# Kernel tuning notes

Hardware: AMD Instinct MI355X
Metric: run time of the kernel (lower is better)

Reference implementation:

```python
import jax, jax.numpy as jnp
import numpy as np

DIL = (1, 2, 4, 8)  # dilations, num_dilation = 4
KS = 3              # kernel_size
EPS = 1e-5


def _unfold3(x, r):
    """nn.Unfold(3, dilation=r, padding=r): x [B,d,H,W] -> [B,d,9,H*W]."""
    B, d, H, W = x.shape
    xp = jnp.pad(x, ((0, 0), (0, 0), (r, r), (r, r)))
    cols = jnp.stack([xp[:, :, i * r:i * r + H, j * r:j * r + W]
                      for i in range(KS) for j in range(KS)], axis=2)
    return cols.reshape(B, d, KS * KS, H * W)


def setup_inputs() -> dict:
    key = jax.random.key(0)
    ks = jax.random.split(key, 8)
    B, C, H, W = 8, 256, 80, 80
    s = 0.05
    return {
        "x": jax.random.normal(ks[0], (B, C, H, W), jnp.float32),
        "qkv_w": jax.random.normal(ks[1], (3 * C, C), jnp.float32) * s,
        "qkv_b": jnp.zeros((3 * C,), jnp.float32),
        "fc_w": jax.random.normal(ks[2], (4, 4), jnp.float32) * 0.3,
        "fc_b": jnp.zeros((4,), jnp.float32),
        "ln_g": jnp.ones((C // 4,), jnp.float32),
        "ln_b": jnp.zeros((C // 4,), jnp.float32),
        "proj_w": jax.random.normal(ks[3], (C, C), jnp.float32) * s,
        "proj_b": jnp.zeros((C,), jnp.float32),
        "w1": jax.random.normal(ks[4], (2 * C, C), jnp.float32) * s,
        "bn1_g": jnp.ones((2 * C,), jnp.float32),
        "bn1_b": jnp.zeros((2 * C,), jnp.float32),
        "bn1_m": jnp.zeros((2 * C,), jnp.float32),
        "bn1_v": jnp.ones((2 * C,), jnp.float32),
        "w2": jax.random.normal(ks[5], (C, 2 * C), jnp.float32) * s,
        "bn2_g": jnp.ones((C,), jnp.float32),
        "bn2_b": jnp.zeros((C,), jnp.float32),
        "bn2_m": jnp.zeros((C,), jnp.float32),
        "bn2_v": jnp.ones((C,), jnp.float32),
    }


def _bn(z, g, b, m, v):
    # BatchNorm2d, eval mode (running stats), z is [B,C,H,W]
    inv = g / jnp.sqrt(v + EPS)
    return z * inv[None, :, None, None] + (b - m * inv)[None, :, None, None]


def _psablock(x, qkv_w, qkv_b, fc_w, fc_b, ln_g, ln_b, proj_w, proj_b,
              w1, bn1_g, bn1_b, bn1_m, bn1_v, w2, bn2_g, bn2_b, bn2_m, bn2_v):
    B, C, H, W = x.shape
    ND = len(DIL)
    Cd = C // ND                  # channels per dilation branch
    num_heads = 4
    hd = C // num_heads           # head_dim = 64
    nh = Cd // hd                 # heads per branch (= 1)
    scale = hd ** -0.5

    # qkv 1x1 conv: [B,3C,H,W] -> (3, ND, Cd) split
    qkv = jnp.einsum('bchw,oc->bohw', x, qkv_w) + qkv_b[None, :, None, None]
    qkv = qkv.reshape(B, 3, ND, Cd, H, W)

    feats = []
    for i, r in enumerate(DIL):
        q, k, v = qkv[:, 0, i], qkv[:, 1, i], qkv[:, 2, i]
        qh = q.reshape(B, nh, hd, H * W)                       # [B,nh,hd,N]
        kh = _unfold3(k, r).reshape(B, nh, hd, KS * KS, H * W)  # [B,nh,hd,9,N]
        vh = _unfold3(v, r).reshape(B, nh, hd, KS * KS, H * W)
        attn = jax.nn.softmax(
            jnp.einsum('bhcn,bhcjn->bhnj', qh, kh) * scale, axis=-1)
        out = jnp.einsum('bhnj,bhcjn->bnhc', attn, vh)          # [B,N,nh,hd]
        feats.append(out.reshape(B, H, W, Cd))

    # CrossScaleFusion: Linear over scale dim + residual + LayerNorm over Cd
    stacked = jnp.stack(feats, axis=3)                          # [B,H,W,S,Cd]
    fused = jnp.einsum('bhwsc,ts->bhwtc', stacked, fc_w) \
        + fc_b[None, None, None, :, None]
    fused = fused + stacked
    mu = fused.mean(-1, keepdims=True)
    var = fused.var(-1, keepdims=True)
    normed = (fused - mu) / jnp.sqrt(var + EPS) * ln_g + ln_b

    y2 = normed.reshape(B, H, W, C)
    y3 = jnp.einsum('bhwc,oc->bhwo', y2, proj_w) + proj_b
    attn_out = y3.transpose(0, 3, 1, 2)                         # [B,C,H,W]

    x1 = x + attn_out                                           # shortcut

    # FFN: Conv1x1(C->2C)+BN+SiLU, Conv1x1(2C->C)+BN, residual
    h = jnp.einsum('bchw,oc->bohw', x1, w1)
    h = jax.nn.silu(_bn(h, bn1_g, bn1_b, bn1_m, bn1_v))
    h = jnp.einsum('bchw,oc->bohw', h, w2)
    h = _bn(h, bn2_g, bn2_b, bn2_m, bn2_v)
    return x1 + h


def reference(x, qkv_w, qkv_b, fc_w, fc_b, ln_g, ln_b, proj_w, proj_b,
              w1, bn1_g, bn1_b, bn1_m, bn1_v, w2, bn2_g, bn2_b, bn2_m, bn2_v):
    return _psablock(x, qkv_w, qkv_b, fc_w, fc_b, ln_g, ln_b, proj_w, proj_b,
                     w1, bn1_g, bn1_b, bn1_m, bn1_v,
                     w2, bn2_g, bn2_b, bn2_m, bn2_v)
```

## Files before the change

kernel.cpp:

```cpp
#include <hip/hip_runtime.h>

#define EPS_F 1e-5f

typedef __attribute__((ext_vector_type(8))) short short8;
typedef __attribute__((ext_vector_type(4))) float f32x4;
typedef __attribute__((ext_vector_type(4))) unsigned short ushort4v;
typedef __attribute__((address_space(1))) void gvoid;
typedef __attribute__((address_space(3))) void svoid;

__device__ __forceinline__ float bf2f(unsigned short u){
    union { unsigned int i; float f; } v; v.i = ((unsigned int)u) << 16; return v.f;
}
__device__ __forceinline__ unsigned short f2bf(float f){
    union { float f; unsigned int i; } v; v.f = f;
    unsigned int r = v.i + 0x7FFFu + ((v.i >> 16) & 1u);
    return (unsigned short)(r >> 16);
}

template<int EPI>
__global__ __launch_bounds__(256, 2)
void mm_k(const short* __restrict__ A, const short* __restrict__ Bt,
          const int M, const int K,
          const float* __restrict__ p0, const float* __restrict__ p1,
          const float* __restrict__ p2, const float* __restrict__ p3,
          const float* __restrict__ resid,
          short* __restrict__ outT, float* __restrict__ outF)
{
    const int N = 6400;
    __shared__ short lsA[128 * 64];
    __shared__ short lsB[128 * 64];

    const int id = blockIdx.x;
    const int b  = id & 7;
    const int rr = id >> 3;
    const int n0 = (rr % 50) * 128;
    const int m0 = (rr / 50) * 128;
    const int t  = threadIdx.x;
    const int l  = t & 63;
    const int w  = t >> 6;
    const int wr = w >> 1, wc = w & 1;

    const short* Bb = Bt + (size_t)b * N * K;

    f32x4 acc[4][4];
    #pragma unroll
    for (int i = 0; i < 4; ++i)
        #pragma unroll
        for (int j = 0; j < 4; ++j) acc[i][j] = (f32x4){0.f, 0.f, 0.f, 0.f};

    const int rsub = l >> 3;
    const int csub = l & 7;

    for (int k0 = 0; k0 < K; k0 += 64) {
        #pragma unroll
        for (int q = 0; q < 4; ++q) {
            const int row = (w * 4 + q) * 8 + rsub;
            const int cs  = csub ^ (row & 7);
            const short* ga = A  + (size_t)(m0 + row) * K + k0 + (cs << 3);
            __builtin_amdgcn_global_load_lds((gvoid*)ga, (svoid*)(lsA + (w * 4 + q) * 512), 16, 0, 0);
            const short* gb = Bb + (size_t)(n0 + row) * K + k0 + (cs << 3);
            __builtin_amdgcn_global_load_lds((gvoid*)gb, (svoid*)(lsB + (w * 4 + q) * 512), 16, 0, 0);
        }
        __syncthreads();

        #pragma unroll
        for (int ks = 0; ks < 2; ++ks) {
            short8 av[4], bv[4];
            const int cfr = ks * 4 + (l >> 4);
            #pragma unroll
            for (int mi = 0; mi < 4; ++mi) {
                const int row = wr * 64 + mi * 16 + (l & 15);
                av[mi] = *(const short8*)&lsA[row * 64 + ((cfr ^ (row & 7)) << 3)];
            }
            #pragma unroll
            for (int ni = 0; ni < 4; ++ni) {
                const int row = wc * 64 + ni * 16 + (l & 15);
                bv[ni] = *(const short8*)&lsB[row * 64 + ((cfr ^ (row & 7)) << 3)];
            }
            #pragma unroll
            for (int mi = 0; mi < 4; ++mi)
                #pragma unroll
                for (int ni = 0; ni < 4; ++ni)
                    acc[mi][ni] = __builtin_amdgcn_mfma_f32_16x16x32_bf16(
                        av[mi], bv[ni], acc[mi][ni], 0, 0, 0);
        }
        __syncthreads();
    }

    const int mq = (l >> 4) * 4;
    const int nq = l & 15;
    #pragma unroll
    for (int mi = 0; mi < 4; ++mi) {
        const int mb = m0 + wr * 64 + mi * 16 + mq;
        float mul[4], add[4];
        #pragma unroll
        for (int j = 0; j < 4; ++j) {
            const int m = mb + j;
            if (EPI == 0 || EPI == 1) { mul[j] = 1.f; add[j] = p0[m]; }
            else { const float inv = p0[m] * rsqrtf(p3[m] + EPS_F);
                   mul[j] = inv; add[j] = p1[m] - p2[m] * inv; }
        }
        #pragma unroll
        for (int ni = 0; ni < 4; ++ni) {
            const int n = n0 + wc * 64 + ni * 16 + nq;
            float z[4];
            #pragma unroll
            for (int j = 0; j < 4; ++j) {
                z[j] = acc[mi][ni][j] * mul[j] + add[j];
                if (EPI == 2) z[j] = z[j] / (1.f + __expf(-z[j]));
                if (EPI == 1 || EPI == 3)
                    z[j] += resid[((size_t)b * M + mb + j) * N + n];
            }
            if (EPI == 0 || EPI == 1 || EPI == 2) {
                ushort4v u;
                #pragma unroll
                for (int j = 0; j < 4; ++j) u[j] = f2bf(z[j]);
                *(ushort4v*)&outT[((size_t)b * N + n) * M + mb] = u;
            }
            if (EPI == 1 || EPI == 3) {
                #pragma unroll
                for (int j = 0; j < 4; ++j)
                    outF[((size_t)b * M + mb + j) * N + n] = z[j];
            }
        }
    }
}

__global__ __launch_bounds__(256, 4)
void attn_k(const short* __restrict__ qkvt,
            const float* __restrict__ fc_w, const float* __restrict__ fc_b,
            const float* __restrict__ ln_g, const float* __restrict__ ln_b,
            short* __restrict__ y2t)
{
    __shared__ short st[4][16][64];

    const int id  = blockIdx.x;
    const int b   = id & 7;
    const int hw0 = (id >> 3) * 16;
    const int t   = threadIdx.x;
    const int px  = t & 15;
    const int cg  = (t >> 4) & 3;
    const int di  = t >> 6;
    const int hw  = hw0 + px;
    const int yy  = hw / 80;
    const int xx  = hw % 80;
    const int r   = 1 << di;

    int   off[9];
    float okf[9];
    #pragma unroll
    for (int jy = 0; jy < 3; ++jy)
        #pragma unroll
        for (int jx = 0; jx < 3; ++jx) {
            const int ny = yy + (jy - 1) * r;
            const int nx = xx + (jx - 1) * r;
            const bool o = (ny >= 0) && (ny < 80) && (nx >= 0) && (nx < 80);
            okf[jy * 3 + jx] = o ? 1.f : 0.f;
            off[jy * 3 + jx] = o ? (ny * 80 + nx) : hw;
        }

    const short* base = qkvt + (size_t)b * 6400 * 768;
    const int ch = di * 64 + cg * 16;

    const short8 qv0 = *(const short8*)(base + (size_t)hw * 768 + ch);
    const short8 qv1 = *(const short8*)(base + (size_t)hw * 768 + ch + 8);
    float qf[16];
    #pragma unroll
    for (int u = 0; u < 8; ++u) { qf[u] = bf2f((unsigned short)qv0[u]);
                                  qf[8 + u] = bf2f((unsigned short)qv1[u]); }

    float s[9];
    #pragma unroll
    for (int j = 0; j < 9; ++j) {
        const short* kp = base + (size_t)off[j] * 768 + 256 + ch;
        const short8 k0 = *(const short8*)kp;
        const short8 k1 = *(const short8*)(kp + 8);
        float a = 0.f;
        #pragma unroll
        for (int u = 0; u < 8; ++u) {
            a = fmaf(qf[u],     bf2f((unsigned short)k0[u]), a);
            a = fmaf(qf[8 + u], bf2f((unsigned short)k1[u]), a);
        }
        s[j] = a;
    }

    #pragma unroll
    for (int j = 0; j < 9; ++j) {
        s[j] += __shfl_xor(s[j], 16, 64);
        s[j] += __shfl_xor(s[j], 32, 64);
        s[j] *= okf[j] * 0.125f;
    }

    float mx = s[0];
    #pragma unroll
    for (int j = 1; j < 9; ++j) mx = fmaxf(mx, s[j]);
    float e[9], sum = 0.f;
    #pragma unroll
    for (int j = 0; j < 9; ++j) { e[j] = __expf(s[j] - mx); sum += e[j]; }
    const float isum = 1.f / sum;
    float pe[9];
    #pragma unroll
    for (int j = 0; j < 9; ++j) pe[j] = e[j] * isum * okf[j];

    float o[16];
    #pragma unroll
    for (int u = 0; u < 16; ++u) o[u] = 0.f;
    #pragma unroll
    for (int j = 0; j < 9; ++j) {
        const short* vp = base + (size_t)off[j] * 768 + 512 + ch;
        const short8 v0 = *(const short8*)vp;
        const short8 v1 = *(const short8*)(vp + 8);
        #pragma unroll
        for (int u = 0; u < 8; ++u) {
            o[u]     = fmaf(pe[j], bf2f((unsigned short)v0[u]), o[u]);
            o[8 + u] = fmaf(pe[j], bf2f((unsigned short)v1[u]), o[8 + u]);
        }
    }
    short8 ov0, ov1;
    #pragma unroll
    for (int u = 0; u < 8; ++u) { ov0[u] = (short)f2bf(o[u]);
                                  ov1[u] = (short)f2bf(o[8 + u]); }
    short* sp = &st[di][px][0];
    *(short8*)(sp + (((cg * 2)     ^ (px & 7)) << 3)) = ov0;
    *(short8*)(sp + (((cg * 2 + 1) ^ (px & 7)) << 3)) = ov1;
    __syncthreads();

    float cw[4];
    #pragma unroll
    for (int s4 = 0; s4 < 4; ++s4) cw[s4] = fc_w[di * 4 + s4] + (s4 == di ? 1.f : 0.f);
    const float fb = fc_b[di];

    const int cc0 = ((cg * 2)     ^ (px & 7)) << 3;
    const int cc1 = ((cg * 2 + 1) ^ (px & 7)) << 3;
    float f[16];
    #pragma unroll
    for (int u = 0; u < 16; ++u) f[u] = fb;
    #pragma unroll
    for (int s4 = 0; s4 < 4; ++s4) {
        const short8 a0 = *(const short8*)(&st[s4][px][0] + cc0);
        const short8 a1 = *(const short8*)(&st[s4][px][0] + cc1);
        #pragma unroll
        for (int u = 0; u < 8; ++u) {
            f[u]     = fmaf(cw[s4], bf2f((unsigned short)a0[u]), f[u]);
            f[8 + u] = fmaf(cw[s4], bf2f((unsigned short)a1[u]), f[8 + u]);
        }
    }
    float mu = 0.f, sq = 0.f;
    #pragma unroll
    for (int u = 0; u < 16; ++u) { mu += f[u]; sq = fmaf(f[u], f[u], sq); }
    mu += __shfl_xor(mu, 16, 64);  mu += __shfl_xor(mu, 32, 64);
    sq += __shfl_xor(sq, 16, 64);  sq += __shfl_xor(sq, 32, 64);
    mu *= (1.f / 64.f);
    const float var  = sq * (1.f / 64.f) - mu * mu;
    const float rstd = rsqrtf(var + EPS_F);

    short* yo = y2t + ((size_t)(b * 6400 + hw)) * 256 + ch;
    short8 y0, y1;
    #pragma unroll
    for (int u = 0; u < 8; ++u) {
        const int c0 = cg * 16 + u, c1 = cg * 16 + 8 + u;
        y0[u] = (short)f2bf((f[u]     - mu) * rstd * ln_g[c0] + ln_b[c0]);
        y1[u] = (short)f2bf((f[8 + u] - mu) * rstd * ln_g[c1] + ln_b[c1]);
    }
    *(short8*)yo       = y0;
    *(short8*)(yo + 8) = y1;
}

__global__ void xt_k(const float* __restrict__ x, short* __restrict__ xt)
{
    const int b  = blockIdx.y;
    const int hw = blockIdx.x * 256 + threadIdx.x;
    const float* xb = x + (size_t)b * 256 * 6400 + hw;
    short* o = xt + ((size_t)b * 6400 + hw) * 256;
    #pragma unroll 4
    for (int c8 = 0; c8 < 32; ++c8) {
        short8 v;
        #pragma unroll
        for (int u = 0; u < 8; ++u)
            v[u] = (short)f2bf(xb[(size_t)(c8 * 8 + u) * 6400]);
        *(short8*)&o[c8 * 8] = v;
    }
}

__global__ void wc_k(const float* __restrict__ a, const float* __restrict__ bb,
                     const float* __restrict__ c, const float* __restrict__ d,
                     short* __restrict__ o)
{
    const int i = blockIdx.x * 256 + threadIdx.x;
    float v;
    if      (i < 196608)  v = a[i];
    else if (i < 262144)  v = bb[i - 196608];
    else if (i < 393216)  v = c[i - 262144];
    else                  v = d[i - 393216];
    o[i] = (short)f2bf(v);
}

extern "C" void kernel_launch(void* const* d_in, const int* in_sizes, int n_in,
                              void* d_out, int out_size, void* d_ws, size_t ws_size,
                              hipStream_t stream)
{
    const float* x      = (const float*)d_in[0];
    const float* qkv_w  = (const float*)d_in[1];
    const float* qkv_b  = (const float*)d_in[2];
    const float* fc_w   = (const float*)d_in[3];
    const float* fc_b   = (const float*)d_in[4];
    const float* ln_g   = (const float*)d_in[5];
    const float* ln_b   = (const float*)d_in[6];
    const float* proj_w = (const float*)d_in[7];
    const float* proj_b = (const float*)d_in[8];
    const float* w1     = (const float*)d_in[9];
    const float* bn1_g  = (const float*)d_in[10];
    const float* bn1_b  = (const float*)d_in[11];
    const float* bn1_m  = (const float*)d_in[12];
    const float* bn1_v  = (const float*)d_in[13];
    const float* w2     = (const float*)d_in[14];
    const float* bn2_g  = (const float*)d_in[15];
    const float* bn2_b  = (const float*)d_in[16];
    const float* bn2_m  = (const float*)d_in[17];
    const float* bn2_v  = (const float*)d_in[18];
    float* out = (float*)d_out;

    const int B = 8;

    char* ws = (char*)d_ws;
    short* wqkvb  = (short*)(ws + 0);
    short* wprojb = wqkvb + 196608;
    short* w1b    = wprojb + 65536;
    short* w2b    = w1b + 131072;
    short* xt     = (short*)(ws + 1048576);
    short* qkvt   = (short*)(ws + 27262976);
    short* y2t    = (short*)(ws + 105906176);
    short* x1t    = (short*)(ws + 132120576);
    float* x1f    = (float*)(ws + 158334976);
    short* h      = qkvt;

    dim3 blk(256);

    wc_k<<<dim3(2048), blk, 0, stream>>>(qkv_w, proj_w, w1, w2, wqkvb);

    xt_k<<<dim3(25, B), blk, 0, stream>>>(x, xt);

    mm_k<0><<<dim3(50 * 6 * 8), blk, 0, stream>>>(
        wqkvb, xt, 768, 256, qkv_b, nullptr, nullptr, nullptr, nullptr,
        qkvt, nullptr);

    attn_k<<<dim3(3200), blk, 0, stream>>>(qkvt, fc_w, fc_b, ln_g, ln_b, y2t);

    mm_k<1><<<dim3(50 * 2 * 8), blk, 0, stream>>>(
        wprojb, y2t, 256, 256, proj_b, nullptr, nullptr, nullptr, x,
        x1t, x1f);

    mm_k<2><<<dim3(50 * 4 * 8), blk, 0, stream>>>(
        w1b, x1t, 512, 256, bn1_g, bn1_b, bn1_m, bn1_v, nullptr,
        h, nullptr);

    mm_k<3><<<dim3(50 * 2 * 8), blk, 0, stream>>>(
        w2b, h, 256, 512, bn2_g, bn2_b, bn2_m, bn2_v, x1f,
        nullptr, out);
}
```

Baseline: 381.7 us.

## Fuse projection GEMM and residual into attention kernel, raise GEMM occupancy

```diff
diff --git a/kernel.cpp b/kernel.cpp
--- a/kernel.cpp
+++ b/kernel.cpp
@@ -18,7 +18,7 @@
 }
 
 template<int EPI>
-__global__ __launch_bounds__(256, 2)
+__global__ __launch_bounds__(256, 3)
 void mm_k(const short* __restrict__ A, const short* __restrict__ Bt,
           const int M, const int K,
           const float* __restrict__ p0, const float* __restrict__ p1,
@@ -96,7 +96,7 @@
         #pragma unroll
         for (int j = 0; j < 4; ++j) {
             const int m = mb + j;
-            if (EPI == 0 || EPI == 1) { mul[j] = 1.f; add[j] = p0[m]; }
+            if (EPI == 0) { mul[j] = 1.f; add[j] = p0[m]; }
             else { const float inv = p0[m] * rsqrtf(p3[m] + EPS_F);
                    mul[j] = inv; add[j] = p1[m] - p2[m] * inv; }
         }
@@ -108,16 +108,16 @@
             for (int j = 0; j < 4; ++j) {
                 z[j] = acc[mi][ni][j] * mul[j] + add[j];
                 if (EPI == 2) z[j] = z[j] / (1.f + __expf(-z[j]));
-                if (EPI == 1 || EPI == 3)
+                if (EPI == 3)
                     z[j] += resid[((size_t)b * M + mb + j) * N + n];
             }
-            if (EPI == 0 || EPI == 1 || EPI == 2) {
+            if (EPI == 0 || EPI == 2) {
                 ushort4v u;
                 #pragma unroll
                 for (int j = 0; j < 4; ++j) u[j] = f2bf(z[j]);
                 *(ushort4v*)&outT[((size_t)b * N + n) * M + mb] = u;
             }
-            if (EPI == 1 || EPI == 3) {
+            if (EPI == 3) {
                 #pragma unroll
                 for (int j = 0; j < 4; ++j)
                     outF[((size_t)b * M + mb + j) * N + n] = z[j];
@@ -127,12 +127,15 @@
 }
 
 __global__ __launch_bounds__(256, 4)
-void attn_k(const short* __restrict__ qkvt,
-            const float* __restrict__ fc_w, const float* __restrict__ fc_b,
-            const float* __restrict__ ln_g, const float* __restrict__ ln_b,
-            short* __restrict__ y2t)
+void atp_k(const short* __restrict__ qkvt,
+           const float* __restrict__ fc_w, const float* __restrict__ fc_b,
+           const float* __restrict__ ln_g, const float* __restrict__ ln_b,
+           const short* __restrict__ wproj, const float* __restrict__ proj_b,
+           const float* __restrict__ x,
+           short* __restrict__ x1t, float* __restrict__ x1f)
 {
     __shared__ short st[4][16][64];
+    __shared__ short y2s[16][256];
 
     const int id  = blockIdx.x;
     const int b   = id & 7;
@@ -183,7 +186,6 @@
         }
         s[j] = a;
     }
-
     #pragma unroll
     for (int j = 0; j < 9; ++j) {
         s[j] += __shfl_xor(s[j], 16, 64);
@@ -254,7 +256,6 @@
     const float var  = sq * (1.f / 64.f) - mu * mu;
     const float rstd = rsqrtf(var + EPS_F);
 
-    short* yo = y2t + ((size_t)(b * 6400 + hw)) * 256 + ch;
     short8 y0, y1;
     #pragma unroll
     for (int u = 0; u < 8; ++u) {
@@ -262,8 +263,49 @@
         y0[u] = (short)f2bf((f[u]     - mu) * rstd * ln_g[c0] + ln_b[c0]);
         y1[u] = (short)f2bf((f[8 + u] - mu) * rstd * ln_g[c1] + ln_b[c1]);
     }
-    *(short8*)yo       = y0;
-    *(short8*)(yo + 8) = y1;
+    {
+        const int cwb = di * 8 + cg * 2;
+        short* yr = &y2s[px][0];
+        *(short8*)(yr + (((cwb)     ^ (px & 7)) << 3)) = y0;
+        *(short8*)(yr + (((cwb + 1) ^ (px & 7)) << 3)) = y1;
+    }
+    __syncthreads();
+
+    const int wv = di;
+    const int kq = (t >> 4) & 3;
+    f32x4 pacc[4];
+    #pragma unroll
+    for (int mi = 0; mi < 4; ++mi) pacc[mi] = (f32x4){0.f, 0.f, 0.f, 0.f};
+
+    #pragma unroll
+    for (int kst = 0; kst < 8; ++kst) {
+        const short8 bY = *(const short8*)&y2s[px][(((kst * 4 + kq) ^ (px & 7)) << 3)];
+        #pragma unroll
+        for (int mi = 0; mi < 4; ++mi) {
+            const int om = wv * 64 + mi * 16 + px;
+            const short8 aW = *(const short8*)&wproj[(size_t)om * 256 + kst * 32 + kq * 8];
+            pacc[mi] = __builtin_amdgcn_mfma_f32_16x16x32_bf16(aW, bY, pacc[mi], 0, 0, 0);
+        }
+    }
+
+    #pragma unroll
+    for (int mi = 0; mi < 4; ++mi) {
+        const int ob = wv * 64 + mi * 16 + kq * 4;
+        float z[4];
+        #pragma unroll
+        for (int j = 0; j < 4; ++j) {
+            const int oc = ob + j;
+            z[j] = pacc[mi][j] + proj_b[oc]
+                 + x[((size_t)(b * 256 + oc)) * 6400 + hw];
+        }
+        ushort4v u;
+        #pragma unroll
+        for (int j = 0; j < 4; ++j) u[j] = f2bf(z[j]);
+        *(ushort4v*)&x1t[((size_t)(b * 6400 + hw)) * 256 + ob] = u;
+        #pragma unroll
+        for (int j = 0; j < 4; ++j)
+            x1f[((size_t)(b * 256 + ob + j)) * 6400 + hw] = z[j];
+    }
 }
 
 __global__ void xt_k(const float* __restrict__ x, short* __restrict__ xt)
@@ -329,7 +371,6 @@
     short* w2b    = w1b + 131072;
     short* xt     = (short*)(ws + 1048576);
     short* qkvt   = (short*)(ws + 27262976);
-    short* y2t    = (short*)(ws + 105906176);
     short* x1t    = (short*)(ws + 132120576);
     float* x1f    = (float*)(ws + 158334976);
     short* h      = qkvt;
@@ -344,11 +385,8 @@
         wqkvb, xt, 768, 256, qkv_b, nullptr, nullptr, nullptr, nullptr,
         qkvt, nullptr);
 
-    attn_k<<<dim3(3200), blk, 0, stream>>>(qkvt, fc_w, fc_b, ln_g, ln_b, y2t);
-
-    mm_k<1><<<dim3(50 * 2 * 8), blk, 0, stream>>>(
-        wprojb, y2t, 256, 256, proj_b, nullptr, nullptr, nullptr, x,
-        x1t, x1f);
+    atp_k<<<dim3(3200), blk, 0, stream>>>(qkvt, fc_w, fc_b, ln_g, ln_b,
+                                          wprojb, proj_b, x, x1t, x1f);
 
     mm_k<2><<<dim3(50 * 4 * 8), blk, 0, stream>>>(
         w1b, x1t, 512, 256, bn1_g, bn1_b, bn1_m, bn1_v, nullptr,
```

Result: slower. 390.8 us (+2.4%).

## Double-buffer B tiles in LDS and load A fragments directly to registers

Applied to the files above, without the earlier changes.

```diff
diff --git a/kernel.cpp b/kernel.cpp
--- a/kernel.cpp
+++ b/kernel.cpp
@@ -16,19 +16,24 @@
     unsigned int r = v.i + 0x7FFFu + ((v.i >> 16) & 1u);
     return (unsigned short)(r >> 16);
 }
-
-template<int EPI>
-__global__ __launch_bounds__(256, 2)
-void mm_k(const short* __restrict__ A, const short* __restrict__ Bt,
-          const int M, const int K,
+__device__ __forceinline__ void blockbar() {
+    __builtin_amdgcn_sched_barrier(0);
+    __builtin_amdgcn_s_barrier();
+    __builtin_amdgcn_sched_barrier(0);
+}
+
+template<int EPI, int KS>
+__global__ __launch_bounds__(256, 3)
+void ga_k(const short* __restrict__ A, const short* __restrict__ Bt,
+          const int M,
           const float* __restrict__ p0, const float* __restrict__ p1,
           const float* __restrict__ p2, const float* __restrict__ p3,
           const float* __restrict__ resid,
           short* __restrict__ outT, float* __restrict__ outF)
 {
     const int N = 6400;
-    __shared__ short lsA[128 * 64];
-    __shared__ short lsB[128 * 64];
+    const int K = KS * 64;
+    __shared__ short lsB[2][128 * 64];
 
     const int id = blockIdx.x;
     const int b  = id & 7;
@@ -41,50 +46,68 @@
     const int wr = w >> 1, wc = w & 1;
 
     const short* Bb = Bt + (size_t)b * N * K;
-
-    f32x4 acc[4][4];
-    #pragma unroll
-    for (int i = 0; i < 4; ++i)
-        #pragma unroll
-        for (int j = 0; j < 4; ++j) acc[i][j] = (f32x4){0.f, 0.f, 0.f, 0.f};
-
     const int rsub = l >> 3;
     const int csub = l & 7;
 
-    for (int k0 = 0; k0 < K; k0 += 64) {
+    auto stageB = [&](int k, int bufi) {
         #pragma unroll
         for (int q = 0; q < 4; ++q) {
             const int row = (w * 4 + q) * 8 + rsub;
             const int cs  = csub ^ (row & 7);
-            const short* ga = A  + (size_t)(m0 + row) * K + k0 + (cs << 3);
-            __builtin_amdgcn_global_load_lds((gvoid*)ga, (svoid*)(lsA + (w * 4 + q) * 512), 16, 0, 0);
-            const short* gb = Bb + (size_t)(n0 + row) * K + k0 + (cs << 3);
-            __builtin_amdgcn_global_load_lds((gvoid*)gb, (svoid*)(lsB + (w * 4 + q) * 512), 16, 0, 0);
-        }
-        __syncthreads();
-
+            const short* gb = Bb + (size_t)(n0 + row) * K + k * 64 + (cs << 3);
+            __builtin_amdgcn_global_load_lds((gvoid*)gb,
+                (svoid*)(&lsB[bufi][(w * 4 + q) * 512]), 16, 0, 0);
+        }
+    };
+
+    const short* Aw = A + (size_t)(m0 + wr * 64 + (l & 15)) * K + ((l >> 4) << 3);
+    short8 areg[2][2][4];
+    auto loadA = [&](int k, int pb) {
+        #pragma unroll
+        for (int ks = 0; ks < 2; ++ks)
+            #pragma unroll
+            for (int mi = 0; mi < 4; ++mi)
+                areg[pb][ks][mi] =
+                    *(const short8*)(Aw + (size_t)mi * 16 * K + k * 64 + ks * 32);
+    };
+
+    f32x4 acc[4][4];
+    #pragma unroll
+    for (int i = 0; i < 4; ++i)
+        #pragma unroll
+        for (int j = 0; j < 4; ++j) acc[i][j] = (f32x4){0.f, 0.f, 0.f, 0.f};
+
+    loadA(0, 0);
+    stageB(0, 0);
+    stageB(1, 1);
+    asm volatile("s_waitcnt vmcnt(4)" ::: "memory");
+    blockbar();
+
+    #pragma unroll
+    for (int k = 0; k < KS; ++k) {
+        if (k + 1 < KS) loadA(k + 1, (k + 1) & 1);
         #pragma unroll
         for (int ks = 0; ks < 2; ++ks) {
-            short8 av[4], bv[4];
+            short8 bv[4];
             const int cfr = ks * 4 + (l >> 4);
-            #pragma unroll
-            for (int mi = 0; mi < 4; ++mi) {
-                const int row = wr * 64 + mi * 16 + (l & 15);
-                av[mi] = *(const short8*)&lsA[row * 64 + ((cfr ^ (row & 7)) << 3)];
-            }
             #pragma unroll
             for (int ni = 0; ni < 4; ++ni) {
                 const int row = wc * 64 + ni * 16 + (l & 15);
-                bv[ni] = *(const short8*)&lsB[row * 64 + ((cfr ^ (row & 7)) << 3)];
+                bv[ni] = *(const short8*)&lsB[k & 1][row * 64 + ((cfr ^ (row & 7)) << 3)];
             }
             #pragma unroll
             for (int mi = 0; mi < 4; ++mi)
                 #pragma unroll
                 for (int ni = 0; ni < 4; ++ni)
                     acc[mi][ni] = __builtin_amdgcn_mfma_f32_16x16x32_bf16(
-                        av[mi], bv[ni], acc[mi][ni], 0, 0, 0);
-        }
-        __syncthreads();
+                        areg[k & 1][ks][mi], bv[ni], acc[mi][ni], 0, 0, 0);
+        }
+        blockbar();
+        if (k + 2 < KS) stageB(k + 2, k & 1);
+        if (k + 1 < KS) {
+            asm volatile("s_waitcnt vmcnt(4)" ::: "memory");
+            blockbar();
+        }
     }
 
     const int mq = (l >> 4) * 4;
@@ -183,7 +206,6 @@
         }
         s[j] = a;
     }
-
     #pragma unroll
     for (int j = 0; j < 9; ++j) {
         s[j] += __shfl_xor(s[j], 16, 64);
@@ -340,21 +362,21 @@
 
     xt_k<<<dim3(25, B), blk, 0, stream>>>(x, xt);
 
-    mm_k<0><<<dim3(50 * 6 * 8), blk, 0, stream>>>(
-        wqkvb, xt, 768, 256, qkv_b, nullptr, nullptr, nullptr, nullptr,
+    ga_k<0, 4><<<dim3(50 * 6 * 8), blk, 0, stream>>>(
+        wqkvb, xt, 768, qkv_b, nullptr, nullptr, nullptr, nullptr,
         qkvt, nullptr);
 
     attn_k<<<dim3(3200), blk, 0, stream>>>(qkvt, fc_w, fc_b, ln_g, ln_b, y2t);
 
-    mm_k<1><<<dim3(50 * 2 * 8), blk, 0, stream>>>(
-        wprojb, y2t, 256, 256, proj_b, nullptr, nullptr, nullptr, x,
+    ga_k<1, 4><<<dim3(50 * 2 * 8), blk, 0, stream>>>(
+        wprojb, y2t, 256, proj_b, nullptr, nullptr, nullptr, x,
         x1t, x1f);
 
-    mm_k<2><<<dim3(50 * 4 * 8), blk, 0, stream>>>(
-        w1b, x1t, 512, 256, bn1_g, bn1_b, bn1_m, bn1_v, nullptr,
+    ga_k<2, 4><<<dim3(50 * 4 * 8), blk, 0, stream>>>(
+        w1b, x1t, 512, bn1_g, bn1_b, bn1_m, bn1_v, nullptr,
         h, nullptr);
 
-    mm_k<3><<<dim3(50 * 2 * 8), blk, 0, stream>>>(
-        w2b, h, 256, 512, bn2_g, bn2_b, bn2_m, bn2_v, x1f,
+    ga_k<3, 8><<<dim3(50 * 2 * 8), blk, 0, stream>>>(
+        w2b, h, 256, bn2_g, bn2_b, bn2_m, bn2_v, x1f,
         nullptr, out);
 }
```

Result: slower. 410.7 us (+7.6%).

## Double-buffer GEMM LDS tiles with K-step 32 and fully unrolled K loop

Applied to the files above, without the earlier changes.

```diff
diff --git a/kernel.cpp b/kernel.cpp
--- a/kernel.cpp
+++ b/kernel.cpp
@@ -17,18 +17,19 @@
     return (unsigned short)(r >> 16);
 }
 
-template<int EPI>
-__global__ __launch_bounds__(256, 2)
-void mm_k(const short* __restrict__ A, const short* __restrict__ Bt,
-          const int M, const int K,
-          const float* __restrict__ p0, const float* __restrict__ p1,
-          const float* __restrict__ p2, const float* __restrict__ p3,
-          const float* __restrict__ resid,
-          short* __restrict__ outT, float* __restrict__ outF)
+template<int EPI, int KS>
+__global__ __launch_bounds__(256, 3)
+void mm2_k(const short* __restrict__ A, const short* __restrict__ Bt,
+           const int M,
+           const float* __restrict__ p0, const float* __restrict__ p1,
+           const float* __restrict__ p2, const float* __restrict__ p3,
+           const float* __restrict__ resid,
+           short* __restrict__ outT, float* __restrict__ outF)
 {
     const int N = 6400;
-    __shared__ short lsA[128 * 64];
-    __shared__ short lsB[128 * 64];
+    const int K = KS * 32;
+    __shared__ short lsA[2][128 * 32];
+    __shared__ short lsB[2][128 * 32];
 
     const int id = blockIdx.x;
     const int b  = id & 7;
@@ -42,40 +43,47 @@
 
     const short* Bb = Bt + (size_t)b * N * K;
 
+    const int srow = t >> 2;
+    const int schk = t & 3;
+
+    auto stage = [&](int k, int bufi) {
+        #pragma unroll
+        for (int q = 0; q < 2; ++q) {
+            const int row = srow + q * 64;
+            const int cs  = schk ^ (row & 3);
+            const short* ga = A  + (size_t)(m0 + row) * K + k * 32 + (cs << 3);
+            __builtin_amdgcn_global_load_lds((gvoid*)ga,
+                (svoid*)(&lsA[bufi][t * 8 + q * 2048]), 16, 0, 0);
+            const short* gb = Bb + (size_t)(n0 + row) * K + k * 32 + (cs << 3);
+            __builtin_amdgcn_global_load_lds((gvoid*)gb,
+                (svoid*)(&lsB[bufi][t * 8 + q * 2048]), 16, 0, 0);
+        }
+    };
+
     f32x4 acc[4][4];
     #pragma unroll
     for (int i = 0; i < 4; ++i)
         #pragma unroll
         for (int j = 0; j < 4; ++j) acc[i][j] = (f32x4){0.f, 0.f, 0.f, 0.f};
 
-    const int rsub = l >> 3;
-    const int csub = l & 7;
-
-    for (int k0 = 0; k0 < K; k0 += 64) {
-        #pragma unroll
-        for (int q = 0; q < 4; ++q) {
-            const int row = (w * 4 + q) * 8 + rsub;
-            const int cs  = csub ^ (row & 7);
-            const short* ga = A  + (size_t)(m0 + row) * K + k0 + (cs << 3);
-            __builtin_amdgcn_global_load_lds((gvoid*)ga, (svoid*)(lsA + (w * 4 + q) * 512), 16, 0, 0);
-            const short* gb = Bb + (size_t)(n0 + row) * K + k0 + (cs << 3);
-            __builtin_amdgcn_global_load_lds((gvoid*)gb, (svoid*)(lsB + (w * 4 + q) * 512), 16, 0, 0);
-        }
-        __syncthreads();
-
-        #pragma unroll
-        for (int ks = 0; ks < 2; ++ks) {
+    stage(0, 0);
+    __syncthreads();
+
+    #pragma unroll
+    for (int k = 0; k < KS; ++k) {
+        if (k + 1 < KS) stage(k + 1, (k + 1) & 1);
+        {
             short8 av[4], bv[4];
-            const int cfr = ks * 4 + (l >> 4);
+            const int cfr = l >> 4;
             #pragma unroll
             for (int mi = 0; mi < 4; ++mi) {
                 const int row = wr * 64 + mi * 16 + (l & 15);
-                av[mi] = *(const short8*)&lsA[row * 64 + ((cfr ^ (row & 7)) << 3)];
+                av[mi] = *(const short8*)&lsA[k & 1][row * 32 + ((cfr ^ (row & 3)) << 3)];
             }
             #pragma unroll
             for (int ni = 0; ni < 4; ++ni) {
                 const int row = wc * 64 + ni * 16 + (l & 15);
-                bv[ni] = *(const short8*)&lsB[row * 64 + ((cfr ^ (row & 7)) << 3)];
+                bv[ni] = *(const short8*)&lsB[k & 1][row * 32 + ((cfr ^ (row & 3)) << 3)];
             }
             #pragma unroll
             for (int mi = 0; mi < 4; ++mi)
@@ -183,7 +191,6 @@
         }
         s[j] = a;
     }
-
     #pragma unroll
     for (int j = 0; j < 9; ++j) {
         s[j] += __shfl_xor(s[j], 16, 64);
@@ -340,21 +347,21 @@
 
     xt_k<<<dim3(25, B), blk, 0, stream>>>(x, xt);
 
-    mm_k<0><<<dim3(50 * 6 * 8), blk, 0, stream>>>(
-        wqkvb, xt, 768, 256, qkv_b, nullptr, nullptr, nullptr, nullptr,
+    mm2_k<0, 8><<<dim3(50 * 6 * 8), blk, 0, stream>>>(
+        wqkvb, xt, 768, qkv_b, nullptr, nullptr, nullptr, nullptr,
         qkvt, nullptr);
 
     attn_k<<<dim3(3200), blk, 0, stream>>>(qkvt, fc_w, fc_b, ln_g, ln_b, y2t);
 
-    mm_k<1><<<dim3(50 * 2 * 8), blk, 0, stream>>>(
-        wprojb, y2t, 256, 256, proj_b, nullptr, nullptr, nullptr, x,
+    mm2_k<1, 8><<<dim3(50 * 2 * 8), blk, 0, stream>>>(
+        wprojb, y2t, 256, proj_b, nullptr, nullptr, nullptr, x,
         x1t, x1f);
 
-    mm_k<2><<<dim3(50 * 4 * 8), blk, 0, stream>>>(
-        w1b, x1t, 512, 256, bn1_g, bn1_b, bn1_m, bn1_v, nullptr,
+    mm2_k<2, 8><<<dim3(50 * 4 * 8), blk, 0, stream>>>(
+        w1b, x1t, 512, bn1_g, bn1_b, bn1_m, bn1_v, nullptr,
         h, nullptr);
 
-    mm_k<3><<<dim3(50 * 2 * 8), blk, 0, stream>>>(
-        w2b, h, 256, 512, bn2_g, bn2_b, bn2_m, bn2_v, x1f,
+    mm2_k<3, 16><<<dim3(50 * 2 * 8), blk, 0, stream>>>(
+        w2b, h, 256, bn2_g, bn2_b, bn2_m, bn2_v, x1f,
         nullptr, out);
 }
```

Result: no change. 375.1 us (-1.7%).
